# Optimization experiments

Hardware: AMD Instinct MI355X
Metric: run time of the kernel (lower is better)

## Reference

```python
import jax, jax.numpy as jnp
import numpy as np

H = 16          # n_head
N = 64          # head_size
LN_EPS = 1e-5 * 8.0 ** 2  # eps * head_size_divisor**2


def _group_norm(x, w, b):
    # x: (B*T, C), H groups of size N, biased variance (torch GroupNorm)
    BT, C = x.shape
    xg = x.reshape(BT, H, C // H)
    m = xg.mean(-1, keepdims=True)
    v = xg.var(-1, keepdims=True)
    xn = (xg - m) / jnp.sqrt(v + LN_EPS)
    return xn.reshape(BT, C) * w + b


def _rwkv7(r, w, k, v, a, b):
    # RWKV-7: S_t = S_{t-1} * diag(exp(-exp(w_t))) + (S_{t-1} a_t) b_t^T + v_t k_t^T ; y_t = S_t r_t
    B, T, C = r.shape
    def rs(z):
        return z.reshape(B, T, H, N).transpose(1, 0, 2, 3)  # (T,B,H,N)
    wd = jnp.exp(-jnp.exp(rs(w)))
    xs = (rs(r), wd, rs(k), rs(v), rs(a), rs(b))
    def step(S, inp):
        rt, wt, kt, vt, at, bt = inp  # each (B,H,N)
        sa = jnp.einsum('bhij,bhj->bhi', S, at)
        S = S * wt[:, :, None, :] + sa[..., None] * bt[:, :, None, :] + vt[..., None] * kt[:, :, None, :]
        return S, jnp.einsum('bhij,bhj->bhi', S, rt)
    S0 = jnp.zeros((B, H, N, N), r.dtype)
    _, y = jax.lax.scan(step, S0, xs)
    return y.transpose(1, 0, 2, 3).reshape(B, T, C)


def setup_inputs():
    key = jax.random.key(0)
    B, T, C = 2, 2048, 1024
    ks = iter(jax.random.split(key, 32))
    def p(shape, s):
        return jax.random.normal(next(ks), shape, jnp.float32) * s
    return {
        'x': p((B, T, C), 1.0),
        'time_maa_x': p((1, 1, C), 0.5), 'time_maa_r': p((1, 1, C), 0.5),
        'time_maa_w': p((1, 1, C), 0.5), 'time_maa_k': p((1, 1, C), 0.5),
        'time_maa_v': p((1, 1, C), 0.5), 'time_maa_a': p((1, 1, C), 0.5),
        'time_maa_g': p((1, 1, C), 0.5),
        'time_decay': p((1, 1, C), 1.0),
        'time_faaaa': p((H, N), 0.1),
        'time_aaaaa': p((1, 1, C), 0.1),
        'time_maa_w1': p((C, 192), 0.02), 'time_maa_w2': p((6, 32, C), 0.02),
        'time_decay_w1': p((C, 64), 0.02), 'time_decay_w2': p((64, C), 0.1),
        'time_aaa_w1': p((C, 64), 0.02), 'time_aaa_w2': p((64, C), 0.1),
        'time_kkk_w1': p((C, 64), 0.02), 'time_kkk_w2': p((64, C), 0.1),
        'gate_w1': p((C, 128), 0.02), 'gate_w2': p((128, C), 0.1),
        'W_r': p((C, C), 0.03), 'W_k': p((C, C), 0.03),
        'W_v': p((C, C), 0.03), 'W_o': p((C, C), 0.03),
        'ln_w': jnp.ones((C,), jnp.float32), 'ln_b': jnp.zeros((C,), jnp.float32),
    }


def reference(x, time_maa_x, time_maa_r, time_maa_w, time_maa_k, time_maa_v,
              time_maa_a, time_maa_g, time_decay, time_faaaa, time_aaaaa,
              time_maa_w1, time_maa_w2, time_decay_w1, time_decay_w2,
              time_aaa_w1, time_aaa_w2, time_kkk_w1, time_kkk_w2,
              gate_w1, gate_w2, W_r, W_k, W_v, W_o, ln_w, ln_b):
    B, T, C = x.shape
    # time_shift: xx[t] = x[t-1] - x[t], x[-1] = 0
    xx = jnp.pad(x, ((0, 0), (1, 0), (0, 0)))[:, :T] - x
    # low-rank token-mix interpolation coefficients (6 branches)
    mix = jnp.tanh((x + xx * time_maa_x) @ time_maa_w1).reshape(B, T, 6, -1)
    m = jnp.einsum('btsd,sdc->sbtc', mix, time_maa_w2)  # (6,B,T,C)
    mr, mw, mk, mv, ma, mg = m[0], m[1], m[2], m[3], m[4], m[5]
    xr = x + xx * (time_maa_r + mr)
    xw = x + xx * (time_maa_w + mw)
    xk = x + xx * (time_maa_k + mk)
    xv = x + xx * (time_maa_v + mv)
    xa = x + xx * (time_maa_a + ma)
    xg = x + xx * (time_maa_g + mg)
    r = xr @ W_r
    w = -jax.nn.softplus(-(time_decay + jnp.tanh(xw @ time_decay_w1) @ time_decay_w2)) - 0.5
    k = xk @ W_k
    v = xv @ W_v
    g = jnp.tanh(xg @ gate_w1) @ gate_w2
    kk = k + jnp.tanh(xk @ time_kkk_w1) @ time_kkk_w2
    kk = kk / jnp.maximum(jnp.linalg.norm(kk, axis=-1, keepdims=True), 1e-12)
    a = jax.nn.sigmoid(time_aaaaa + (xa @ time_aaa_w1) @ time_aaa_w2) * 2.0
    k = k * jnp.exp(jnp.minimum(w * 0.5, 0.0))
    y = _rwkv7(r, w, k, v, -kk, kk * a)
    y = _group_norm(y.reshape(B * T, C), ln_w, ln_b).reshape(B, T, C)
    rh = r.reshape(B, T, H, N)
    kh = k.reshape(B, T, H, N)
    vh = v.reshape(B, T, H, N)
    bonus = ((rh * kh * time_faaaa).sum(-1, keepdims=True) * vh).reshape(B, T, C)
    y = y + bonus
    return (y * g) @ W_o
```

## Files before the change

kernel.cpp:

```cpp
#include <hip/hip_runtime.h>
#include <hip/hip_bf16.h>

using bf16 = __hip_bfloat16;
using bf16x8 = __attribute__((ext_vector_type(8))) short;
using f32x4 = __attribute__((ext_vector_type(4))) float;

#define B_ 2
#define T_ 2048
#define C_ 1024
#define BT_ (B_*T_)
#define H_ 16
#define N_ 64
#define LCH 32
#define NCH (T_/LCH)
#define CHD (B_*H_*NCH)

__device__ __forceinline__ float allred64(float v) {
#pragma unroll
  for (int m = 1; m < 64; m <<= 1) v += __shfl_xor(v, m, 64);
  return v;
}

__device__ __forceinline__ bf16 tobf(float f) { return __float2bfloat16(f); }
__device__ __forceinline__ float frombf(bf16 b) { return __bfloat162float(b); }
__device__ __forceinline__ float bf2f(unsigned short u) {
  unsigned int x = ((unsigned int)u) << 16;
  return __builtin_bit_cast(float, x);
}
__device__ __forceinline__ unsigned short bfbits(float f) {
  return __builtin_bit_cast(unsigned short, __float2bfloat16(f));
}
__device__ __forceinline__ float rdlane(float v, int m) {
  return __builtin_bit_cast(float,
      __builtin_amdgcn_readlane(__builtin_bit_cast(int, v), m));
}

__device__ __forceinline__ f32x4 mfma16x16x32(bf16x8 a, bf16x8 b, f32x4 c) {
  return __builtin_amdgcn_mfma_f32_16x16x32_bf16(a, b, c, 0, 0, 0);
}

typedef const __attribute__((address_space(1))) unsigned int* gas_ptr;
typedef __attribute__((address_space(3))) unsigned int* las_ptr;
__device__ __forceinline__ void gload16(const void* g, void* l) {
  __builtin_amdgcn_global_load_lds((gas_ptr)g, (las_ptr)l, 16, 0, 0);
}

__global__ void ws_diag(float a, float b, float* out) { out[0] = a; out[1] = b; }

struct PrepArgs {
  const float* src[19];
  bf16* dst[19];
};
__constant__ int kTR[19] = {1024,1024,1024,1024, 1024, 32,32,32,32,32,32,
                            1024,64, 1024,64, 1024,64, 1024,128};
__constant__ int kTC[19] = {1024,1024,1024,1024, 192, 1024,1024,1024,1024,1024,1024,
                            64,1024, 64,1024, 64,1024, 128,1024};

__global__ __launch_bounds__(256) void prep_weights(PrepArgs pa) {
  const int job = blockIdx.y;
  const int R = kTR[job], Cc = kTC[job];
  const int ntx = Cc >> 5, nty = R >> 5;
  const int tile = blockIdx.x;
  if (tile >= ntx * nty) return;
  const int tx = tile % ntx, ty = tile / ntx;
  const float* __restrict__ src = pa.src[job];
  bf16* __restrict__ dst = pa.dst[job];
  __shared__ float tl[32][33];
  const int lx = threadIdx.x & 31, ly = threadIdx.x >> 5;
#pragma unroll
  for (int q = 0; q < 4; ++q)
    tl[ly + 8*q][lx] = src[(size_t)(ty*32 + ly + 8*q) * Cc + tx*32 + lx];
  __syncthreads();
#pragma unroll
  for (int q = 0; q < 4; ++q)
    dst[(size_t)(tx*32 + ly + 8*q) * R + ty*32 + lx] = tobf(tl[lx][ly + 8*q]);
}

template<int EPI>
__global__ __launch_bounds__(256) void gemm_bt(
    const bf16* __restrict__ A, int lda,
    const bf16* __restrict__ Bt, int ldb,
    void* __restrict__ Cout, int ldc, int K)
{
  __shared__ short As[64][40];
  __shared__ short Bs[64][40];
  const int bm0 = blockIdx.x * 64;
  const int bn0 = blockIdx.y * 64;
  const int tid = threadIdx.x;
  const int wave = tid >> 6, lane = tid & 63;
  const int lm = lane & 15, kg = lane >> 4;
  const int srow = tid >> 2, scol = (tid & 3) * 8;
  f32x4 acc[4] = {};
  const size_t abase = (size_t)(bm0 + srow) * lda + scol;
  const size_t bbase = (size_t)(bn0 + srow) * ldb + scol;
  for (int k0 = 0; k0 < K; k0 += 32) {
    *(uint4*)&As[srow][scol] = *(const uint4*)(A + abase + k0);
    *(uint4*)&Bs[srow][scol] = *(const uint4*)(Bt + bbase + k0);
    __syncthreads();
    bf16x8 af = *(const bf16x8*)&As[wave*16 + lm][kg*8];
#pragma unroll
    for (int f = 0; f < 4; ++f) {
      bf16x8 bfr = *(const bf16x8*)&Bs[f*16 + lm][kg*8];
      acc[f] = mfma16x16x32(af, bfr, acc[f]);
    }
    __syncthreads();
  }
  const int row0 = bm0 + wave*16 + kg*4;
  const int col0 = bn0 + lm;
#pragma unroll
  for (int f = 0; f < 4; ++f) {
#pragma unroll
    for (int q = 0; q < 4; ++q) {
      float val = acc[f][q];
      size_t o = (size_t)(row0 + q) * ldc + col0 + f*16;
      if (EPI == 0)      ((float*)Cout)[o] = val;
      else if (EPI == 1) ((bf16*)Cout)[o] = tobf(tanhf(val));
      else               ((bf16*)Cout)[o] = tobf(val);
    }
  }
}

struct Proj4Args { const bf16* A[4]; const bf16* Bt[4]; bf16* out[4];
                   int N[4]; int tnh[4]; };
__global__ __launch_bounds__(256) void proj4(Proj4Args p4) {
  const int z = blockIdx.z;
  const int Nn = p4.N[z];
  const int bn0 = blockIdx.y * 64;
  if (bn0 >= Nn) return;
  __shared__ short As[64][40];
  __shared__ short Bs[64][40];
  const bf16* __restrict__ A  = p4.A[z];
  const bf16* __restrict__ Bt = p4.Bt[z];
  bf16* __restrict__ out = p4.out[z];
  const int tnh = p4.tnh[z];
  const int bm0 = blockIdx.x * 64;
  const int tid = threadIdx.x;
  const int wave = tid >> 6, lane = tid & 63;
  const int lm = lane & 15, kg = lane >> 4;
  const int srow = tid >> 2, scol = (tid & 3) * 8;
  f32x4 acc[4] = {};
  const size_t abase = (size_t)(bm0 + srow) * C_ + scol;
  const size_t bbase = (size_t)(bn0 + srow) * C_ + scol;
  for (int k0 = 0; k0 < C_; k0 += 32) {
    *(uint4*)&As[srow][scol] = *(const uint4*)(A + abase + k0);
    *(uint4*)&Bs[srow][scol] = *(const uint4*)(Bt + bbase + k0);
    __syncthreads();
    bf16x8 af = *(const bf16x8*)&As[wave*16 + lm][kg*8];
#pragma unroll
    for (int f = 0; f < 4; ++f) {
      bf16x8 bfr = *(const bf16x8*)&Bs[f*16 + lm][kg*8];
      acc[f] = mfma16x16x32(af, bfr, acc[f]);
    }
    __syncthreads();
  }
  const int row0 = bm0 + wave*16 + kg*4;
  const int col0 = bn0 + lm;
#pragma unroll
  for (int f = 0; f < 4; ++f) {
#pragma unroll
    for (int q = 0; q < 4; ++q) {
      float val = acc[f][q];
      size_t o = (size_t)(row0 + q) * Nn + col0 + f*16;
      out[o] = tobf(tnh ? tanhf(val) : val);
    }
  }
}

template<int EPI>
__global__ __launch_bounds__(256) void gemm128(
    const bf16* __restrict__ A, int lda,
    const bf16* __restrict__ Bt, int ldb,
    void* __restrict__ Cout, int ldc, int K,
    const float* __restrict__ aux1, bf16* __restrict__ aux2)
{
  __shared__ bf16 As[128][32];
  __shared__ bf16 Bs[128][32];
  const int bm0 = blockIdx.x * 128, bn0 = blockIdx.y * 128;
  const int tid = threadIdx.x, wv = tid >> 6, ln = tid & 63;
  const int wr = wv >> 1, wc = wv & 1;
  const int lm = ln & 15, kg = ln >> 4;
  const int srow = ln >> 2, scol = (ln & 3) * 8;
  f32x4 acc[4][4] = {};
  for (int k0 = 0; k0 < K; k0 += 32) {
#pragma unroll
    for (int i = 0; i < 2; ++i) {
      const int r0 = wv*32 + i*16;
      gload16(A  + (size_t)(bm0 + r0 + srow) * lda + k0 + scol, &As[r0][0]);
      gload16(Bt + (size_t)(bn0 + r0 + srow) * ldb + k0 + scol, &Bs[r0][0]);
    }
    asm volatile("s_waitcnt vmcnt(0)" ::: "memory");
    __syncthreads();
    bf16x8 af[4], bfr[4];
#pragma unroll
    for (int m = 0; m < 4; ++m) af[m] = *(const bf16x8*)&As[wr*64 + m*16 + lm][kg*8];
#pragma unroll
    for (int n = 0; n < 4; ++n) bfr[n] = *(const bf16x8*)&Bs[wc*64 + n*16 + lm][kg*8];
#pragma unroll
    for (int m = 0; m < 4; ++m)
#pragma unroll
      for (int n = 0; n < 4; ++n)
        acc[m][n] = mfma16x16x32(af[m], bfr[n], acc[m][n]);
    __syncthreads();
  }
#pragma unroll
  for (int m = 0; m < 4; ++m) {
    const int row0 = bm0 + wr*64 + m*16 + kg*4;
#pragma unroll
    for (int n = 0; n < 4; ++n) {
      const int col = bn0 + wc*64 + n*16 + lm;
#pragma unroll
      for (int q = 0; q < 4; ++q) {
        float val = acc[m][n][q];
        size_t o = (size_t)(row0 + q) * ldc + col;
        if (EPI == 0)      ((float*)Cout)[o] = val;
        else if (EPI == 2) ((bf16*)Cout)[o] = tobf(val);
        else if (EPI == 3) {
          float wr2 = val + aux1[col];
          float sp = fmaxf(-wr2, 0.f) + log1pf(expf(-fabsf(wr2)));
          float w = -sp - 0.5f;
          ((bf16*)Cout)[o] = tobf(-expf(w));
          aux2[o] = tobf(frombf(aux2[o]) * expf(fminf(0.5f*w, 0.f)));
        } else if (EPI == 4) {
          float z = aux1[col] + val;
          ((bf16*)Cout)[o] = tobf(2.f / (1.f + expf(-z)));
        }
      }
    }
  }
}

struct RkvArgs { const bf16* A[3]; const bf16* Bt[3]; bf16* Cq[3]; };
__global__ __launch_bounds__(256) void gemm128_rkv(RkvArgs ra) {
  __shared__ bf16 As[128][32];
  __shared__ bf16 Bs[128][32];
  const bf16* __restrict__ A  = ra.A[blockIdx.z];
  const bf16* __restrict__ Bt = ra.Bt[blockIdx.z];
  bf16* __restrict__ Cout = ra.Cq[blockIdx.z];
  const int bm0 = blockIdx.x * 128, bn0 = blockIdx.y * 128;
  const int tid = threadIdx.x, wv = tid >> 6, ln = tid & 63;
  const int wr = wv >> 1, wc = wv & 1;
  const int lm = ln & 15, kg = ln >> 4;
  const int srow = ln >> 2, scol = (ln & 3) * 8;
  f32x4 acc[4][4] = {};
  for (int k0 = 0; k0 < C_; k0 += 32) {
#pragma unroll
    for (int i = 0; i < 2; ++i) {
      const int r0 = wv*32 + i*16;
      gload16(A  + (size_t)(bm0 + r0 + srow) * C_ + k0 + scol, &As[r0][0]);
      gload16(Bt + (size_t)(bn0 + r0 + srow) * C_ + k0 + scol, &Bs[r0][0]);
    }
    asm volatile("s_waitcnt vmcnt(0)" ::: "memory");
    __syncthreads();
    bf16x8 af[4], bfr[4];
#pragma unroll
    for (int m = 0; m < 4; ++m) af[m] = *(const bf16x8*)&As[wr*64 + m*16 + lm][kg*8];
#pragma unroll
    for (int n = 0; n < 4; ++n) bfr[n] = *(const bf16x8*)&Bs[wc*64 + n*16 + lm][kg*8];
#pragma unroll
    for (int m = 0; m < 4; ++m)
#pragma unroll
      for (int n = 0; n < 4; ++n)
        acc[m][n] = mfma16x16x32(af[m], bfr[n], acc[m][n]);
    __syncthreads();
  }
#pragma unroll
  for (int m = 0; m < 4; ++m) {
    const int row0 = bm0 + wr*64 + m*16 + kg*4;
#pragma unroll
    for (int n = 0; n < 4; ++n) {
      const int col = bn0 + wc*64 + n*16 + lm;
#pragma unroll
      for (int q = 0; q < 4; ++q)
        Cout[(size_t)(row0 + q) * C_ + col] = tobf(acc[m][n][q]);
    }
  }
}

struct Mix6Args { const float* maa[6]; bf16* out[6]; };

__global__ __launch_bounds__(256) void mix_combine(
    const bf16* __restrict__ mixb, const bf16* __restrict__ w2t,
    const bf16* __restrict__ xb, Mix6Args ma)
{
  __shared__ short As[64][40];
  __shared__ short Bs[64][40];
  const int s6 = blockIdx.z;
  const bf16* __restrict__ A  = mixb + s6*32;
  const bf16* __restrict__ Bt = w2t + (size_t)s6*C_*32;
  const float* __restrict__ maa = ma.maa[s6];
  bf16* __restrict__ out = ma.out[s6];
  const int bm0 = blockIdx.x * 64, bn0 = blockIdx.y * 64;
  const int tid = threadIdx.x, wave = tid >> 6, lane = tid & 63;
  const int lm = lane & 15, kg = lane >> 4;
  const int srow = tid >> 2, scol = (tid & 3) * 8;
  *(uint4*)&As[srow][scol] = *(const uint4*)(A + (size_t)(bm0 + srow)*192 + scol);
  *(uint4*)&Bs[srow][scol] = *(const uint4*)(Bt + (size_t)(bn0 + srow)*32 + scol);
  __syncthreads();
  bf16x8 af = *(const bf16x8*)&As[wave*16 + lm][kg*8];
  f32x4 acc[4] = {};
#pragma unroll
  for (int f = 0; f < 4; ++f) {
    bf16x8 bfr = *(const bf16x8*)&Bs[f*16 + lm][kg*8];
    acc[f] = mfma16x16x32(af, bfr, acc[f]);
  }
  const int row0 = bm0 + wave*16 + kg*4;
  const int col0 = bn0 + lm;
#pragma unroll
  for (int f = 0; f < 4; ++f) {
#pragma unroll
    for (int q = 0; q < 4; ++q) {
      const int row = row0 + q, col = col0 + f*16;
      const size_t o = (size_t)row * C_ + col;
      float xv = frombf(xb[o]);
      float xp = (row & (T_ - 1)) ? frombf(xb[o - C_]) : 0.f;
      out[o] = tobf(xv + (xp - xv) * (maa[col] + acc[f][q]));
    }
  }
}

__global__ __launch_bounds__(256) void xin_k(
    const float* __restrict__ x, const float* __restrict__ maa_x,
    bf16* __restrict__ xinb, bf16* __restrict__ xb)
{
  size_t idx = (size_t)blockIdx.x * 256 + threadIdx.x;
  int c = idx & (C_ - 1);
  int t = (int)((idx >> 10) & (T_ - 1));
  float xv = x[idx];
  float xp = t ? x[idx - C_] : 0.f;
  xinb[idx] = tobf(xv + (xp - xv) * maa_x[c]);
  xb[idx] = tobf(xv);
}

__global__ __launch_bounds__(256) void kk_normalize(
    const bf16* __restrict__ kraw, const bf16* __restrict__ kkadd,
    bf16* __restrict__ kkout)
{
  const int bt = blockIdx.x;
  const int tid = threadIdx.x;
  const size_t o = (size_t)bt * C_;
  float vals[4]; float ss = 0.f;
#pragma unroll
  for (int q = 0; q < 4; ++q) {
    float u = frombf(kraw[o + tid + q*256]) + frombf(kkadd[o + tid + q*256]);
    vals[q] = u; ss += u * u;
  }
  ss = allred64(ss);
  __shared__ float red[4];
  const int wave = tid >> 6, lane = tid & 63;
  if (lane == 0) red[wave] = ss;
  __syncthreads();
  float tot = red[0] + red[1] + red[2] + red[3];
  float inv = 1.f / fmaxf(sqrtf(tot), 1e-12f);
#pragma unroll
  for (int q = 0; q < 4; ++q) kkout[o + tid + q*256] = tobf(vals[q] * inv);
}


__global__ __launch_bounds__(256, 3) void rwkv_chunk_pre(
    const bf16* __restrict__ rr, const bf16* __restrict__ lw,
    const bf16* __restrict__ kk_s, const bf16* __restrict__ kkv,
    const bf16* __restrict__ aam, const bf16* __restrict__ vv,
    bf16* __restrict__ wbufb, bf16* __restrict__ sabufb,
    bf16* __restrict__ abybufb, bf16* __restrict__ ckybufb,
    bf16* __restrict__ ubufP, bf16* __restrict__ mbufT)
{
  __shared__ float Am[LCH][33], Cm[LCH][33];
  __shared__ float wtot[4][64];
  __shared__ float lcl[64];
  __shared__ bf16 bTb[LCH][72], kTb[LCH][72], vLb[LCH][72];
  __shared__ bf16 bTT[64][40], kTT[64][40], vLT[64][40];
  __shared__ bf16 uni[5120];
  bf16 (*aCb)[72] = (bf16(*)[72])uni;
  bf16 (*rCb)[72] = (bf16(*)[72])(uni + 2304);
  bf16 (*WT)[40]  = (bf16(*)[40])uni;
  bf16 (*SAT)[40] = (bf16(*)[40])(uni + 2560);

  const int ch = blockIdx.x;
  const int c  = ch & (NCH - 1);
  const int bh = ch >> 6;
  const int b  = bh >> 4, h = bh & 15;
  const int tid = threadIdx.x, wv = tid >> 6, ln = tid & 63;
  const int lm = ln & 15, kg = ln >> 4;
  const size_t base = ((size_t)(b*T_ + c*LCH) * C_) + h*N_ + ln;

  float lwr[8], lcE[8];
  {
    float run = 0.f;
#pragma unroll
    for (int q = 0; q < 8; ++q) {
      lwr[q] = frombf(lw[base + (size_t)(wv*8 + q) * C_]);
      lcE[q] = run; run += lwr[q];
    }
    wtot[wv][ln] = run;
  }
  __syncthreads();
  {
    float pre = 0.f;
    for (int w2 = 0; w2 < wv; ++w2) pre += wtot[w2][ln];
    if (wv == 0) lcl[ln] = wtot[0][ln] + wtot[1][ln] + wtot[2][ln] + wtot[3][ln];
#pragma unroll
    for (int q = 0; q < 8; ++q) lcE[q] += pre;
  }
#pragma unroll
  for (int q = 0; q < 8; ++q) {
    const int s = wv*8 + q;
    const size_t off = base + (size_t)s * C_;
    float kkx = frombf(kkv[off]), aax = frombf(aam[off]);
    float kx = frombf(kk_s[off]), rx = frombf(rr[off]);
    float lcI = lcE[q] + lwr[q];
    float eIm = __expf(-lcI);
    float av = -kkx * __expf(lcE[q]);
    float bv = kkx * aax * eIm;
    float kv2 = kx * eIm;
    float rv = rx * __expf(lcI);
    bf16 vxb = vv[off];
    aCb[s][ln] = tobf(av);  rCb[s][ln] = tobf(rv);
    bTb[s][ln] = tobf(bv);  kTb[s][ln] = tobf(kv2);
    vLb[s][ln] = vxb;
    bTT[ln][s] = tobf(bv);  kTT[ln][s] = tobf(kv2);  vLT[ln][s] = vxb;
  }
  __syncthreads();

  {
    const bf16 (*Ab)[72] = (wv < 2) ? aCb : rCb;
    const bf16 (*Bb)[72] = (wv & 1) ? kTb : bTb;
#pragma unroll
    for (int mt = 0; mt < 2; ++mt)
#pragma unroll
      for (int nt = 0; nt < 2; ++nt) {
        f32x4 acc = {};
#pragma unroll
        for (int ks = 0; ks < 2; ++ks) {
          bf16x8 af = *(const bf16x8*)&Ab[mt*16 + lm][ks*32 + kg*8];
          bf16x8 bq = *(const bf16x8*)&Bb[nt*16 + lm][ks*32 + kg*8];
          acc = mfma16x16x32(af, bq, acc);
        }
        const int row0 = mt*16 + kg*4, col = nt*16 + lm;
#pragma unroll
        for (int q = 0; q < 4; ++q) {
          float v = acc[q];
          if (wv == 0)      Am[row0+q][col] = v;
          else if (wv == 1) Cm[row0+q][col] = v;
          else {
            bf16 bv2 = tobf(col <= row0+q ? v : 0.f);
            if (wv == 2) abybufb[(size_t)ch*1024 + (row0+q)*32 + col] = bv2;
            else         ckybufb[(size_t)ch*1024 + (row0+q)*32 + col] = bv2;
          }
        }
      }
  }
  __syncthreads();

  float Xr[32], amr[32];
  if (wv == 0) {
#pragma unroll
    for (int s = 0; s < 32; ++s) amr[s] = Am[s][ln & 31];
#pragma unroll
    for (int s = 0; s < 32; ++s) Xr[s] = frombf(aCb[s][ln]);
  } else if (wv == 1) {
    float cmr[32];
#pragma unroll
    for (int s = 0; s < 32; ++s) { amr[s] = Am[s][ln & 31]; cmr[s] = Cm[s][ln & 31]; }
#pragma unroll
    for (int s = 0; s < 32; ++s) Xr[s] = 0.f;
#pragma unroll
    for (int u = 0; u < 31; ++u) {
      float v = frombf(vLb[u][ln]);
#pragma unroll
      for (int s = u + 1; s < 32; ++s) Xr[s] += rdlane(cmr[s], u) * v;
    }
  }
  __syncthreads();

  if (wv < 2) {
#pragma unroll
    for (int s = 1; s < 32; ++s) {
      float acc = Xr[s];
#pragma unroll
      for (int u = 0; u < s; ++u) acc += rdlane(amr[s], u) * Xr[u];
      Xr[s] = acc;
    }
    if (wv == 0) {
#pragma unroll
      for (int s = 0; s < 32; ++s) {
        bf16 bv = tobf(Xr[s]);
        WT[ln][s] = bv;
        wbufb[(size_t)ch*2048 + s*64 + ln] = bv;
      }
    } else {
#pragma unroll
      for (int s = 0; s < 32; ++s) {
        bf16 bv = tobf(Xr[s]);
        SAT[ln][s] = bv;
        sabufb[(size_t)ch*2048 + s*64 + ln] = bv;
      }
    }
  }
  __syncthreads();

  {
    const int mt = wv;
    bf16x8 aS = *(const bf16x8*)&SAT[mt*16 + lm][kg*8];
    bf16x8 aV = *(const bf16x8*)&vLT[mt*16 + lm][kg*8];
    bf16x8 aW = *(const bf16x8*)&WT[mt*16 + lm][kg*8];
#pragma unroll
    for (int nt = 0; nt < 4; ++nt) {
      bf16x8 bB = *(const bf16x8*)&bTT[nt*16 + lm][kg*8];
      bf16x8 bK = *(const bf16x8*)&kTT[nt*16 + lm][kg*8];
      f32x4 aU = {}, aG = {};
      aU = mfma16x16x32(aS, bB, aU);
      aU = mfma16x16x32(aV, bK, aU);
      aG = mfma16x16x32(aW, bB, aG);
      const int i0r = mt*16 + kg*4, col = nt*16 + lm;
      float dl = __expf(lcl[col]);
      uint2 up;
      up.x = (unsigned int)bfbits(aU[0]*dl) | ((unsigned int)bfbits(aU[1]*dl) << 16);
      up.y = (unsigned int)bfbits(aU[2]*dl) | ((unsigned int)bfbits(aU[3]*dl) << 16);
      *(uint2*)(ubufP + (size_t)ch*4096 + (mt*4 + nt)*256 + ln*4) = up;
      float m0 = (aG[0] + (i0r+0 == col ? 1.f : 0.f)) * dl;
      float m1 = (aG[1] + (i0r+1 == col ? 1.f : 0.f)) * dl;
      float m2 = (aG[2] + (i0r+2 == col ? 1.f : 0.f)) * dl;
      float m3 = (aG[3] + (i0r+3 == col ? 1.f : 0.f)) * dl;
      uint2 mp;
      mp.x = (unsigned int)bfbits(m0) | ((unsigned int)bfbits(m1) << 16);
      mp.y = (unsigned int)bfbits(m2) | ((unsigned int)bfbits(m3) << 16);
      const int laned = (((mt*2) + (kg >> 1)) & 3) * 16 + lm;
      *(uint2*)(mbufT + (size_t)ch*4096 + (nt*2 + (mt >> 1))*512
                + laned*8 + (kg & 1)*4) = mp;
    }
  }
}

__global__ __launch_bounds__(256) void rwkv_chunk_state(
    const bf16* __restrict__ mbufT, const bf16* __restrict__ ubufP,
    bf16* __restrict__ s0bufb)
{
  __shared__ bf16 Sst[4][16][72];
  const int bh = blockIdx.x;
  const int tid = threadIdx.x, wv = tid >> 6, ln = tid & 63;
  const int lm = ln & 15, kg = ln >> 4;

#pragma unroll
  for (int r = 0; r < 16; ++r) {
    Sst[wv][r][ln] = tobf(0.f);
    if (ln < 8) Sst[wv][r][64 + ln] = tobf(0.f);
  }

  bf16x8 BfA[4][2], BfB[4][2];
  uint2 UpA[4], UpB[4];
  auto prefetch = [&](bf16x8 (&Bf)[4][2], uint2 (&Up)[4], int c) {
    const size_t chp = (size_t)(bh*NCH + c) * 4096;
#pragma unroll
    for (int nt = 0; nt < 4; ++nt) {
      Bf[nt][0] = *(const bf16x8*)(mbufT + chp + (nt*2 + 0)*512 + ln*8);
      Bf[nt][1] = *(const bf16x8*)(mbufT + chp + (nt*2 + 1)*512 + ln*8);
      Up[nt]    = *(const uint2*) (ubufP + chp + (wv*4 + nt)*256 + ln*4);
    }
  };
  prefetch(BfA, UpA, 0);
  prefetch(BfB, UpB, 1);

  auto body = [&](bf16x8 (&Bf)[4][2], uint2 (&Up)[4], int c) {
    const size_t ch4 = (size_t)(bh*NCH + c) * 4096;
    const int sr = ln >> 2, sc = (ln & 3) * 16;
    uint4 v0 = *(const uint4*)&Sst[wv][sr][sc];
    uint4 v1 = *(const uint4*)&Sst[wv][sr][sc + 8];
    *(uint4*)(s0bufb + ch4 + (size_t)(wv*16 + sr)*64 + sc) = v0;
    *(uint4*)(s0bufb + ch4 + (size_t)(wv*16 + sr)*64 + sc + 8) = v1;
    bf16x8 A0 = *(const bf16x8*)&Sst[wv][lm][kg*8];
    bf16x8 A1 = *(const bf16x8*)&Sst[wv][lm][32 + kg*8];
    f32x4 acc[4];
#pragma unroll
    for (int nt = 0; nt < 4; ++nt) {
      acc[nt][0] = bf2f((unsigned short)(Up[nt].x & 0xffff));
      acc[nt][1] = bf2f((unsigned short)(Up[nt].x >> 16));
      acc[nt][2] = bf2f((unsigned short)(Up[nt].y & 0xffff));
      acc[nt][3] = bf2f((unsigned short)(Up[nt].y >> 16));
      acc[nt] = mfma16x16x32(A0, Bf[nt][0], acc[nt]);
      acc[nt] = mfma16x16x32(A1, Bf[nt][1], acc[nt]);
    }
    int cp = c + 2; if (cp > NCH - 1) cp = NCH - 1;
    prefetch(Bf, Up, cp);
#pragma unroll
    for (int nt = 0; nt < 4; ++nt)
#pragma unroll
      for (int q = 0; q < 4; ++q)
        Sst[wv][kg*4 + q][nt*16 + lm] = tobf(acc[nt][q]);
  };

  for (int cc = 0; cc < NCH; cc += 2) {
    body(BfA, UpA, cc);
    body(BfB, UpB, cc + 1);
  }
}

__global__ __launch_bounds__(256, 4) void rwkv_chunk_out(
    const bf16* __restrict__ rr, const bf16* __restrict__ lw,
    const bf16* __restrict__ vv, const bf16* __restrict__ kks,
    const bf16* __restrict__ gg, const bf16* __restrict__ s0bufb,
    const bf16* __restrict__ wbufb, const bf16* __restrict__ sabufb,
    const bf16* __restrict__ abybufb, const bf16* __restrict__ ckybufb,
    const float* __restrict__ faaaa, const float* __restrict__ lnw,
    const float* __restrict__ lnb, bf16* __restrict__ zb)
{
  __shared__ bf16 S0b[64][72];
  __shared__ bf16 ABl[LCH][40], CKl[LCH][40];
  __shared__ bf16 SAot[64][40], VlT[64][40];
  __shared__ float wtot[4][64];
  __shared__ float bonus[LCH];
  __shared__ float uni2f[2304];
  bf16 (*Wb)[72]  = (bf16(*)[72])uni2f;
  bf16 (*Rlb)[72] = (bf16(*)[72])((bf16*)uni2f + 2304);
  float (*Yl)[68] = (float(*)[68])uni2f;

  const int ch = blockIdx.x;
  const int c = ch & (NCH - 1), bh = ch >> 6, b = bh >> 4, h = bh & 15;
  const int tid = threadIdx.x, wv = tid >> 6, ln = tid & 63;
  const int lm = ln & 15, kg = ln >> 4;
  const size_t base = ((size_t)(b*T_ + c*LCH) * C_) + h*N_ + ln;

  float lwr[8], lcE[8];
  {
    float run = 0.f;
#pragma unroll
    for (int q = 0; q < 8; ++q) {
      lwr[q] = frombf(lw[base + (size_t)(wv*8 + q) * C_]);
      lcE[q] = run; run += lwr[q];
    }
    wtot[wv][ln] = run;
  }
  __syncthreads();
  {
    float pre = 0.f;
    for (int w2 = 0; w2 < wv; ++w2) pre += wtot[w2][ln];
#pragma unroll
    for (int q = 0; q < 8; ++q) lcE[q] += pre;
  }
  const float fa = faaaa[h*N_ + ln];
#pragma unroll
  for (int q = 0; q < 8; ++q) {
    const int s = wv*8 + q;
    const size_t off = base + (size_t)s * C_;
    float rf = frombf(rr[off]);
    Rlb[s][ln] = tobf(rf * __expf(lcE[q] + lwr[q]));
    VlT[ln][s] = vv[off];
    float rk = allred64(rf * frombf(kks[off]) * fa);
    if (ln == 0) bonus[s] = rk;
  }
#pragma unroll
  for (int t = 0; t < 2; ++t) {
    int cc2 = tid*2 + t; int ri = cc2 >> 3, co = (cc2 & 7) * 8;
    *(uint4*)&S0b[ri][co] = *(const uint4*)(s0bufb + (size_t)ch*4096 + ri*64 + co);
  }
  { int ri = tid >> 3, co = (tid & 7) * 8;
    *(uint4*)&Wb[ri][co] = *(const uint4*)(wbufb + (size_t)ch*2048 + ri*64 + co); }
  if (tid < 128) {
    int ri = tid >> 2, co = (tid & 3) * 8;
    *(uint4*)&ABl[ri][co] = *(const uint4*)(abybufb + (size_t)ch*1024 + ri*32 + co);
  } else {
    int t2 = tid - 128; int ri = t2 >> 2, co = (t2 & 3) * 8;
    *(uint4*)&CKl[ri][co] = *(const uint4*)(ckybufb + (size_t)ch*1024 + ri*32 + co);
  }
  __syncthreads();

  const int mt = wv >> 1, ntb = (wv & 1) * 2;
#pragma unroll
  for (int t = 0; t < 2; ++t) {
    const int nt = ntb + t;
    const int row0 = mt*16 + kg*4, col = nt*16 + lm;
    f32x4 acc;
#pragma unroll
    for (int q = 0; q < 4; ++q)
      acc[q] = frombf(sabufb[(size_t)ch*2048 + (row0+q)*64 + col]);
#pragma unroll
    for (int ks = 0; ks < 2; ++ks) {
      bf16x8 af = *(const bf16x8*)&Wb[mt*16 + lm][ks*32 + kg*8];
      bf16x8 bq = *(const bf16x8*)&S0b[nt*16 + lm][ks*32 + kg*8];
      acc = mfma16x16x32(af, bq, acc);
    }
#pragma unroll
    for (int q = 0; q < 4; ++q) SAot[col][row0+q] = tobf(acc[q]);
  }
  __syncthreads();

  f32x4 yacc[2];
#pragma unroll
  for (int t = 0; t < 2; ++t) {
    const int nt = ntb + t;
    f32x4 acc = {};
#pragma unroll
    for (int ks = 0; ks < 2; ++ks) {
      bf16x8 af = *(const bf16x8*)&Rlb[mt*16 + lm][ks*32 + kg*8];
      bf16x8 bq = *(const bf16x8*)&S0b[nt*16 + lm][ks*32 + kg*8];
      acc = mfma16x16x32(af, bq, acc);
    }
    {
      bf16x8 af = *(const bf16x8*)&ABl[mt*16 + lm][kg*8];
      bf16x8 bq = *(const bf16x8*)&SAot[nt*16 + lm][kg*8];
      acc = mfma16x16x32(af, bq, acc);
    }
    {
      bf16x8 af = *(const bf16x8*)&CKl[mt*16 + lm][kg*8];
      bf16x8 bq = *(const bf16x8*)&VlT[nt*16 + lm][kg*8];
      acc = mfma16x16x32(af, bq, acc);
    }
    yacc[t] = acc;
  }
  __syncthreads();

#pragma unroll
  for (int t = 0; t < 2; ++t) {
    const int nt = ntb + t;
    const int row0 = mt*16 + kg*4, col = nt*16 + lm;
#pragma unroll
    for (int q = 0; q < 4; ++q) Yl[row0 + q][col] = yacc[t][q];
  }
  __syncthreads();

  {
    const int s2 = tid >> 3, c0 = (tid & 7) * 8;
    float yv[8]; float sum = 0.f;
#pragma unroll
    for (int i = 0; i < 8; ++i) { yv[i] = Yl[s2][c0 + i]; sum += yv[i]; }
#pragma unroll
    for (int m = 1; m < 8; m <<= 1) sum += __shfl_xor(sum, m, 64);
    const float mean = sum * (1.f/64.f);
    float ss = 0.f;
#pragma unroll
    for (int i = 0; i < 8; ++i) { float d = yv[i] - mean; ss += d * d; }
#pragma unroll
    for (int m = 1; m < 8; m <<= 1) ss += __shfl_xor(ss, m, 64);
    const float inv = rsqrtf(ss * (1.f/64.f) + 6.4e-4f);
    const float bn = bonus[s2];
    const size_t trow = (size_t)(b*T_ + c*LCH + s2) * C_ + h*N_ + c0;
    bf16 zout[8];
#pragma unroll
    for (int i = 0; i < 8; ++i) {
      const int col = c0 + i, cidx = h*N_ + col;
      float gn = (yv[i] - mean) * inv * lnw[cidx] + lnb[cidx];
      float z = (gn + bn * frombf(VlT[col][s2])) * frombf(gg[trow + i - trow % 1]);
      zout[i] = tobf(z);
    }
#pragma unroll
    for (int i = 0; i < 8; ++i) {
      float gn = (yv[i] - mean) * inv * lnw[h*N_ + c0 + i] + lnb[h*N_ + c0 + i];
      float z = (gn + bn * frombf(VlT[c0 + i][s2])) * frombf(gg[trow + i]);
      zout[i] = tobf(z);
    }
    *(uint4*)(zb + trow) = *(const uint4*)&zout[0];
  }
}

extern "C" void kernel_launch(void* const* d_in, const int* in_sizes, int n_in,
                              void* d_out, int out_size, void* d_ws, size_t ws_size,
                              hipStream_t stream)
{
  const float* x     = (const float*)d_in[0];
  const float* maa_x = (const float*)d_in[1];
  const float* maa_r = (const float*)d_in[2];
  const float* maa_w = (const float*)d_in[3];
  const float* maa_k = (const float*)d_in[4];
  const float* maa_v = (const float*)d_in[5];
  const float* maa_a = (const float*)d_in[6];
  const float* maa_g = (const float*)d_in[7];
  const float* tdec  = (const float*)d_in[8];
  const float* faaaa = (const float*)d_in[9];
  const float* aaaaa = (const float*)d_in[10];
  const float* maa_w1= (const float*)d_in[11];
  const float* maa_w2= (const float*)d_in[12];
  const float* dec_w1= (const float*)d_in[13];
  const float* dec_w2= (const float*)d_in[14];
  const float* aaa_w1= (const float*)d_in[15];
  const float* aaa_w2= (const float*)d_in[16];
  const float* kkk_w1= (const float*)d_in[17];
  const float* kkk_w2= (const float*)d_in[18];
  const float* gate_w1=(const float*)d_in[19];
  const float* gate_w2=(const float*)d_in[20];
  const float* W_r   = (const float*)d_in[21];
  const float* W_k   = (const float*)d_in[22];
  const float* W_v   = (const float*)d_in[23];
  const float* W_o   = (const float*)d_in[24];
  const float* lnw   = (const float*)d_in[25];
  const float* lnb   = (const float*)d_in[26];

  char* ws = (char*)d_ws;
  size_t cur = 0;
  auto alloc = [&](size_t bytes) -> void* {
    void* p = ws + cur; cur += (bytes + 255) & ~(size_t)255; return p;
  };
  const size_t HBT = (size_t)BT_ * C_ * 2;

  bf16* rb   = (bf16*)alloc(HBT);
  bf16* kb   = (bf16*)alloc(HBT);
  bf16* vb   = (bf16*)alloc(HBT);
  bf16* gbb  = (bf16*)alloc(HBT);
  bf16* WtR  = (bf16*)alloc((size_t)C_*C_*2);
  bf16* WtK  = (bf16*)alloc((size_t)C_*C_*2);
  bf16* WtV  = (bf16*)alloc((size_t)C_*C_*2);
  bf16* WtO  = (bf16*)alloc((size_t)C_*C_*2);
  bf16* w1t  = (bf16*)alloc((size_t)192*C_*2);
  bf16* w2t  = (bf16*)alloc((size_t)6*C_*32*2);
  bf16* d1t  = (bf16*)alloc((size_t)64*C_*2);
  bf16* d2t  = (bf16*)alloc((size_t)C_*64*2);
  bf16* a1t  = (bf16*)alloc((size_t)64*C_*2);
  bf16* a2t  = (bf16*)alloc((size_t)C_*64*2);
  bf16* k1t  = (bf16*)alloc((size_t)64*C_*2);
  bf16* k2t  = (bf16*)alloc((size_t)C_*64*2);
  bf16* g1t  = (bf16*)alloc((size_t)128*C_*2);
  bf16* g2t  = (bf16*)alloc((size_t)C_*128*2);
  bf16* lwb  = (bf16*)alloc(HBT);
  bf16* kkb  = (bf16*)alloc(HBT);
  bf16* aamt = (bf16*)alloc(HBT);
  bf16* s0bufb = kkb;

  const size_t ubase = cur;
  bf16* mtmpb = (bf16*)alloc(HBT);
  bf16* xinb = (bf16*)alloc(HBT);
  bf16* xb   = (bf16*)alloc(HBT);
  bf16* mixb = (bf16*)alloc((size_t)BT_*192*2);
  bf16* xbr[6];
  for (int s = 0; s < 6; ++s) xbr[s] = (bf16*)alloc(HBT);
  bf16* h64k = (bf16*)alloc((size_t)BT_*64*2);
  bf16* h64d = (bf16*)alloc((size_t)BT_*64*2);
  bf16* h64a = (bf16*)alloc((size_t)BT_*64*2);
  bf16* h128b= (bf16*)alloc((size_t)BT_*128*2);
  const size_t tmp_end = cur;
  cur = ubase;
  bf16*  wbufb   = (bf16*)alloc((size_t)CHD*2048*2);
  bf16*  sabufb  = (bf16*)alloc((size_t)CHD*2048*2);
  bf16*  abybufb = (bf16*)alloc((size_t)CHD*1024*2);
  bf16*  ckybufb = (bf16*)alloc((size_t)CHD*1024*2);
  bf16*  ubufP   = (bf16*)alloc((size_t)CHD*4096*2);
  bf16*  mbufT   = (bf16*)alloc((size_t)CHD*4096*2);
  bf16*  zb      = (bf16*)ubufP;
  if (tmp_end > cur) cur = tmp_end;
  const size_t need = cur;
  (void)in_sizes; (void)n_in; (void)out_size;

  if (ws_size < need) {
    ws_diag<<<1, 1, 0, stream>>>((float)ws_size, (float)need, (float*)d_out);
    return;
  }

  PrepArgs pa;
  pa.src[0] = W_r;  pa.dst[0] = WtR;
  pa.src[1] = W_k;  pa.dst[1] = WtK;
  pa.src[2] = W_v;  pa.dst[2] = WtV;
  pa.src[3] = W_o;  pa.dst[3] = WtO;
  pa.src[4] = maa_w1; pa.dst[4] = w1t;
  for (int s = 0; s < 6; ++s) { pa.src[5+s] = maa_w2 + (size_t)s*32*C_; pa.dst[5+s] = w2t + (size_t)s*C_*32; }
  pa.src[11] = dec_w1; pa.dst[11] = d1t;
  pa.src[12] = dec_w2; pa.dst[12] = d2t;
  pa.src[13] = aaa_w1; pa.dst[13] = a1t;
  pa.src[14] = aaa_w2; pa.dst[14] = a2t;
  pa.src[15] = kkk_w1; pa.dst[15] = k1t;
  pa.src[16] = kkk_w2; pa.dst[16] = k2t;
  pa.src[17] = gate_w1; pa.dst[17] = g1t;
  pa.src[18] = gate_w2; pa.dst[18] = g2t;
  prep_weights<<<dim3(1024, 19), 256, 0, stream>>>(pa);

  const int EW_GRID = (BT_ * C_) / 256;
  xin_k<<<EW_GRID, 256, 0, stream>>>(x, maa_x, xinb, xb);

  gemm_bt<1><<<dim3(64, 3), 256, 0, stream>>>(xinb, C_, w1t, C_, mixb, 192, C_);

  Mix6Args ma;
  ma.maa[0] = maa_r; ma.maa[1] = maa_w; ma.maa[2] = maa_k;
  ma.maa[3] = maa_v; ma.maa[4] = maa_a; ma.maa[5] = maa_g;
  for (int s = 0; s < 6; ++s) ma.out[s] = xbr[s];
  mix_combine<<<dim3(64, 16, 6), 256, 0, stream>>>(mixb, w2t, xb, ma);

  RkvArgs ra;
  ra.A[0] = xbr[0]; ra.Bt[0] = WtR; ra.Cq[0] = rb;
  ra.A[1] = xbr[2]; ra.Bt[1] = WtK; ra.Cq[1] = kb;
  ra.A[2] = xbr[3]; ra.Bt[2] = WtV; ra.Cq[2] = vb;
  gemm128_rkv<<<dim3(32, 8, 3), 256, 0, stream>>>(ra);

  Proj4Args p4;
  p4.A[0] = xbr[2]; p4.Bt[0] = k1t; p4.out[0] = h64k; p4.N[0] = 64;  p4.tnh[0] = 1;
  p4.A[1] = xbr[1]; p4.Bt[1] = d1t; p4.out[1] = h64d; p4.N[1] = 64;  p4.tnh[1] = 1;
  p4.A[2] = xbr[4]; p4.Bt[2] = a1t; p4.out[2] = h64a; p4.N[2] = 64;  p4.tnh[2] = 0;
  p4.A[3] = xbr[5]; p4.Bt[3] = g1t; p4.out[3] = h128b; p4.N[3] = 128; p4.tnh[3] = 1;
  proj4<<<dim3(64, 2, 4), 256, 0, stream>>>(p4);

  gemm128<2><<<dim3(32, 8), 256, 0, stream>>>(h64k, 64, k2t, 64, mtmpb, C_, 64, nullptr, nullptr);
  kk_normalize<<<BT_, 256, 0, stream>>>(kb, mtmpb, kkb);

  gemm128<3><<<dim3(32, 8), 256, 0, stream>>>(h64d, 64, d2t, 64, lwb, C_, 64, tdec, kb);

  gemm128<4><<<dim3(32, 8), 256, 0, stream>>>(h64a, 64, a2t, 64, aamt, C_, 64, aaaaa, nullptr);

  gemm128<2><<<dim3(32, 8), 256, 0, stream>>>(h128b, 128, g2t, 128, gbb, C_, 128, nullptr, nullptr);

  rwkv_chunk_pre<<<CHD, 256, 0, stream>>>(rb, lwb, kb, kkb, aamt, vb,
      wbufb, sabufb, abybufb, ckybufb, ubufP, mbufT);
  rwkv_chunk_state<<<32, 256, 0, stream>>>(mbufT, ubufP, s0bufb);
  rwkv_chunk_out<<<CHD, 256, 0, stream>>>(rb, lwb, vb, kb, gbb, s0bufb,
      wbufb, sabufb, abybufb, ckybufb, faaaa, lnw, lnb, zb);

  gemm128<0><<<dim3(32, 8), 256, 0, stream>>>(zb, C_, WtO, C_, d_out, C_, C_, nullptr, nullptr);
}
```

Before: 311.7 us.

## Batch four LoRA up-projection GEMMs into one launch and trim chunk-kernel exps

Merges the four separate small-K GEMM launches (kkk, decay, aaa, gate) into a single z-indexed kernel with per-slice epilogues. The decay epilogue now writes scaled k into a new buffer, so that slice no longer updates kb in place while the kkk slice reads it, and downstream kernels read the new buffer. In the chunk precompute it replaces one exp with a reciprocal and hoists the per-column decay exp into shared memory. It also deletes a duplicated output loop in the chunk-output kernel. The point is fewer kernel launches, better GPU fill from the larger grid, and less transcendental work, at the cost of an extra activation-sized buffer and a runtime epilogue branch.

```diff
diff --git a/kernel.cpp b/kernel.cpp
--- a/kernel.cpp
+++ b/kernel.cpp
@@ -170,8 +170,7 @@
 __global__ __launch_bounds__(256) void gemm128(
     const bf16* __restrict__ A, int lda,
     const bf16* __restrict__ Bt, int ldb,
-    void* __restrict__ Cout, int ldc, int K,
-    const float* __restrict__ aux1, bf16* __restrict__ aux2)
+    void* __restrict__ Cout, int ldc, int K)
 {
   __shared__ bf16 As[128][32];
   __shared__ bf16 Bs[128][32];
@@ -212,18 +211,8 @@
       for (int q = 0; q < 4; ++q) {
         float val = acc[m][n][q];
         size_t o = (size_t)(row0 + q) * ldc + col;
-        if (EPI == 0)      ((float*)Cout)[o] = val;
-        else if (EPI == 2) ((bf16*)Cout)[o] = tobf(val);
-        else if (EPI == 3) {
-          float wr2 = val + aux1[col];
-          float sp = fmaxf(-wr2, 0.f) + log1pf(expf(-fabsf(wr2)));
-          float w = -sp - 0.5f;
-          ((bf16*)Cout)[o] = tobf(-expf(w));
-          aux2[o] = tobf(frombf(aux2[o]) * expf(fminf(0.5f*w, 0.f)));
-        } else if (EPI == 4) {
-          float z = aux1[col] + val;
-          ((bf16*)Cout)[o] = tobf(2.f / (1.f + expf(-z)));
-        }
+        if (EPI == 0) ((float*)Cout)[o] = val;
+        else          ((bf16*)Cout)[o] = tobf(val);
       }
     }
   }
@@ -272,6 +261,75 @@
 #pragma unroll
       for (int q = 0; q < 4; ++q)
         Cout[(size_t)(row0 + q) * C_ + col] = tobf(acc[m][n][q]);
+    }
+  }
+}
+
+struct Ep4Args {
+  const bf16* A[4]; const bf16* Bt[4]; bf16* Cout[4];
+  int K[4]; int epi[4];
+  const float* aux[4];
+  const bf16* kin; bf16* ksout;
+};
+__global__ __launch_bounds__(256) void gemm128_ep4(Ep4Args ea) {
+  __shared__ bf16 As[128][32];
+  __shared__ bf16 Bs[128][32];
+  const int z = blockIdx.z;
+  const bf16* __restrict__ A  = ea.A[z];
+  const bf16* __restrict__ Bt = ea.Bt[z];
+  bf16* __restrict__ Cout = ea.Cout[z];
+  const int K = ea.K[z], epi = ea.epi[z];
+  const float* __restrict__ aux = ea.aux[z];
+  const int bm0 = blockIdx.x * 128, bn0 = blockIdx.y * 128;
+  const int tid = threadIdx.x, wv = tid >> 6, ln = tid & 63;
+  const int wr = wv >> 1, wc = wv & 1;
+  const int lm = ln & 15, kg = ln >> 4;
+  const int srow = ln >> 2, scol = (ln & 3) * 8;
+  f32x4 acc[4][4] = {};
+  for (int k0 = 0; k0 < K; k0 += 32) {
+#pragma unroll
+    for (int i = 0; i < 2; ++i) {
+      const int r0 = wv*32 + i*16;
+      gload16(A  + (size_t)(bm0 + r0 + srow) * K + k0 + scol, &As[r0][0]);
+      gload16(Bt + (size_t)(bn0 + r0 + srow) * K + k0 + scol, &Bs[r0][0]);
+    }
+    asm volatile("s_waitcnt vmcnt(0)" ::: "memory");
+    __syncthreads();
+    bf16x8 af[4], bfr[4];
+#pragma unroll
+    for (int m = 0; m < 4; ++m) af[m] = *(const bf16x8*)&As[wr*64 + m*16 + lm][kg*8];
+#pragma unroll
+    for (int n = 0; n < 4; ++n) bfr[n] = *(const bf16x8*)&Bs[wc*64 + n*16 + lm][kg*8];
+#pragma unroll
+    for (int m = 0; m < 4; ++m)
+#pragma unroll
+      for (int n = 0; n < 4; ++n)
+        acc[m][n] = mfma16x16x32(af[m], bfr[n], acc[m][n]);
+    __syncthreads();
+  }
+#pragma unroll
+  for (int m = 0; m < 4; ++m) {
+    const int row0 = bm0 + wr*64 + m*16 + kg*4;
+#pragma unroll
+    for (int n = 0; n < 4; ++n) {
+      const int col = bn0 + wc*64 + n*16 + lm;
+#pragma unroll
+      for (int q = 0; q < 4; ++q) {
+        float val = acc[m][n][q];
+        size_t o = (size_t)(row0 + q) * C_ + col;
+        if (epi == 2) {
+          Cout[o] = tobf(val);
+        } else if (epi == 4) {
+          float zz = aux[col] + val;
+          Cout[o] = tobf(2.f / (1.f + expf(-zz)));
+        } else {
+          float wr2 = val + aux[col];
+          float sp = fmaxf(-wr2, 0.f) + log1pf(expf(-fabsf(wr2)));
+          float w = -sp - 0.5f;
+          Cout[o] = tobf(-expf(w));
+          ea.ksout[o] = tobf(frombf(ea.kin[o]) * expf(fminf(0.5f*w, 0.f)));
+        }
+      }
     }
   }
 }
@@ -367,6 +425,7 @@
   __shared__ float Am[LCH][33], Cm[LCH][33];
   __shared__ float wtot[4][64];
   __shared__ float lcl[64];
+  __shared__ float dll[64];
   __shared__ bf16 bTb[LCH][72], kTb[LCH][72], vLb[LCH][72];
   __shared__ bf16 bTT[64][40], kTT[64][40], vLT[64][40];
   __shared__ bf16 uni[5120];
@@ -409,10 +468,11 @@
     float kx = frombf(kk_s[off]), rx = frombf(rr[off]);
     float lcI = lcE[q] + lwr[q];
     float eIm = __expf(-lcI);
+    float eI  = __builtin_amdgcn_rcpf(eIm);
     float av = -kkx * __expf(lcE[q]);
     float bv = kkx * aax * eIm;
     float kv2 = kx * eIm;
-    float rv = rx * __expf(lcI);
+    float rv = rx * eI;
     bf16 vxb = vv[off];
     aCb[s][ln] = tobf(av);  rCb[s][ln] = tobf(rv);
     bTb[s][ln] = tobf(bv);  kTb[s][ln] = tobf(kv2);
@@ -420,6 +480,7 @@
     bTT[ln][s] = tobf(bv);  kTT[ln][s] = tobf(kv2);  vLT[ln][s] = vxb;
   }
   __syncthreads();
+  if (tid < 64) dll[tid] = __expf(lcl[tid]);
 
   {
     const bf16 (*Ab)[72] = (wv < 2) ? aCb : rCb;
@@ -512,7 +573,7 @@
       aU = mfma16x16x32(aV, bK, aU);
       aG = mfma16x16x32(aW, bB, aG);
       const int i0r = mt*16 + kg*4, col = nt*16 + lm;
-      float dl = __expf(lcl[col]);
+      float dl = dll[col];
       uint2 up;
       up.x = (unsigned int)bfbits(aU[0]*dl) | ((unsigned int)bfbits(aU[1]*dl) << 16);
       up.y = (unsigned int)bfbits(aU[2]*dl) | ((unsigned int)bfbits(aU[3]*dl) << 16);
@@ -734,13 +795,6 @@
     const float bn = bonus[s2];
     const size_t trow = (size_t)(b*T_ + c*LCH + s2) * C_ + h*N_ + c0;
     bf16 zout[8];
-#pragma unroll
-    for (int i = 0; i < 8; ++i) {
-      const int col = c0 + i, cidx = h*N_ + col;
-      float gn = (yv[i] - mean) * inv * lnw[cidx] + lnb[cidx];
-      float z = (gn + bn * frombf(VlT[col][s2])) * frombf(gg[trow + i - trow % 1]);
-      zout[i] = tobf(z);
-    }
 #pragma unroll
     for (int i = 0; i < 8; ++i) {
       float gn = (yv[i] - mean) * inv * lnw[h*N_ + c0 + i] + lnb[h*N_ + c0 + i];
@@ -792,6 +846,7 @@
 
   bf16* rb   = (bf16*)alloc(HBT);
   bf16* kb   = (bf16*)alloc(HBT);
+  bf16* ksb  = (bf16*)alloc(HBT);
   bf16* vb   = (bf16*)alloc(HBT);
   bf16* gbb  = (bf16*)alloc(HBT);
   bf16* WtR  = (bf16*)alloc((size_t)C_*C_*2);
@@ -883,20 +938,21 @@
   p4.A[3] = xbr[5]; p4.Bt[3] = g1t; p4.out[3] = h128b; p4.N[3] = 128; p4.tnh[3] = 1;
   proj4<<<dim3(64, 2, 4), 256, 0, stream>>>(p4);
 
-  gemm128<2><<<dim3(32, 8), 256, 0, stream>>>(h64k, 64, k2t, 64, mtmpb, C_, 64, nullptr, nullptr);
+  Ep4Args ea;
+  ea.A[0] = h64k;  ea.Bt[0] = k2t; ea.Cout[0] = mtmpb; ea.K[0] = 64;  ea.epi[0] = 2; ea.aux[0] = nullptr;
+  ea.A[1] = h64d;  ea.Bt[1] = d2t; ea.Cout[1] = lwb;   ea.K[1] = 64;  ea.epi[1] = 5; ea.aux[1] = tdec;
+  ea.A[2] = h64a;  ea.Bt[2] = a2t; ea.Cout[2] = aamt;  ea.K[2] = 64;  ea.epi[2] = 4; ea.aux[2] = aaaaa;
+  ea.A[3] = h128b; ea.Bt[3] = g2t; ea.Cout[3] = gbb;   ea.K[3] = 128; ea.epi[3] = 2; ea.aux[3] = nullptr;
+  ea.kin = kb; ea.ksout = ksb;
+  gemm128_ep4<<<dim3(32, 8, 4), 256, 0, stream>>>(ea);
+
   kk_normalize<<<BT_, 256, 0, stream>>>(kb, mtmpb, kkb);
 
-  gemm128<3><<<dim3(32, 8), 256, 0, stream>>>(h64d, 64, d2t, 64, lwb, C_, 64, tdec, kb);
-
-  gemm128<4><<<dim3(32, 8), 256, 0, stream>>>(h64a, 64, a2t, 64, aamt, C_, 64, aaaaa, nullptr);
-
-  gemm128<2><<<dim3(32, 8), 256, 0, stream>>>(h128b, 128, g2t, 128, gbb, C_, 128, nullptr, nullptr);
-
-  rwkv_chunk_pre<<<CHD, 256, 0, stream>>>(rb, lwb, kb, kkb, aamt, vb,
+  rwkv_chunk_pre<<<CHD, 256, 0, stream>>>(rb, lwb, ksb, kkb, aamt, vb,
       wbufb, sabufb, abybufb, ckybufb, ubufP, mbufT);
   rwkv_chunk_state<<<32, 256, 0, stream>>>(mbufT, ubufP, s0bufb);
-  rwkv_chunk_out<<<CHD, 256, 0, stream>>>(rb, lwb, vb, kb, gbb, s0bufb,
+  rwkv_chunk_out<<<CHD, 256, 0, stream>>>(rb, lwb, vb, ksb, gbb, s0bufb,
       wbufb, sabufb, abybufb, ckybufb, faaaa, lnw, lnb, zb);
 
-  gemm128<0><<<dim3(32, 8), 256, 0, stream>>>(zb, C_, WtO, C_, d_out, C_, C_, nullptr, nullptr);
-}
+  gemm128<0><<<dim3(32, 8), 256, 0, stream>>>(zb, C_, WtO, C_, d_out, C_, C_);
+}
```

Measured after the change: 307.6 us. Within noise of the previous version (-1.3%).
